# Kernel tuning notes

Measured on AMD Instinct MI355X. Metric: run time of the kernel, lower is better.

## Reference

```python
import jax, jax.numpy as jnp
import numpy as np

_SAMPLING_EPS = 1e-5


def setup_inputs() -> dict:
    key = jax.random.key(0)
    k1, k2, k3, k4, k5 = jax.random.split(key, 5)
    B, V = 128, 128000
    logits = jax.random.normal(k1, (B, V), dtype=jnp.float32)
    temperature = jax.random.uniform(k2, (B,), dtype=jnp.float32)
    top_k = jax.random.randint(k3, (B,), 0, 1024)
    top_p = jax.random.uniform(k4, (B,), dtype=jnp.float32)
    # uniform noise -> exponential via -log(u) inside reference (torch's q.exponential_())
    q = jnp.clip(jax.random.uniform(k5, (B, V), dtype=jnp.float32), 1e-10, 1.0)
    return {"logits": logits, "temperature": temperature, "top_k": top_k,
            "top_p": top_p, "q": q, "max_num_logprobs": 5}


def reference(logits, temperature, top_k, top_p, q, max_num_logprobs):
    B, V = logits.shape
    # apply_temperature: temp < eps treated as 1.0 (greedy rows untouched)
    temp = jnp.where(temperature < _SAMPLING_EPS, 1.0, temperature)
    logits = logits.astype(jnp.float32) / temp[:, None]

    # _apply_top_k_top_p: ascending sort over vocab
    idx = jnp.argsort(logits, axis=-1)                      # [B, V]
    ls = jnp.take_along_axis(logits, idx, axis=-1)          # sorted ascending
    k = jnp.clip(top_k.astype(jnp.int32), 1, V)
    thr = jnp.take_along_axis(ls, (V - k)[:, None], axis=-1)  # k-th largest value
    ls = jnp.where(ls < thr, -jnp.inf, ls)
    # top-p on the top-k-masked sorted logits
    ps = jax.nn.softmax(ls, axis=-1)
    cum = jnp.cumsum(ps, axis=-1)
    p_mask = cum <= (1.0 - top_p)[:, None]
    p_mask = p_mask.at[:, -1].set(False)
    ls = jnp.where(p_mask, -jnp.inf, ls)
    # scatter masked sorted logits back to original vocab positions
    rows = jnp.arange(B)[:, None]
    logits = jnp.zeros_like(logits).at[rows, idx].set(ls)

    # get_probs + sample
    probs = jax.nn.softmax(logits, axis=-1)
    e = -jnp.log(q)                                         # exponential noise
    greedy = jnp.argmax(probs, axis=-1)
    rand = jnp.argmax(probs / e, axis=-1)                   # Gumbel-max equivalent
    sampled = jnp.where(temperature < _SAMPLING_EPS, greedy, rand).astype(jnp.int32)

    # top-k logprobs
    logprobs = jax.nn.log_softmax(logits, axis=-1)
    topk_logprobs, topk_indices = jax.lax.top_k(logprobs, max_num_logprobs)
    return sampled, topk_logprobs, topk_indices.astype(jnp.int32)
```

## Files before the change

kernel.cpp:

```cpp
#include <hip/hip_runtime.h>
#include <math.h>
#include <float.h>

typedef unsigned long long u64;
typedef unsigned u32;

#define NT 1024
#define NW 16
#define NT1 256
#define SL 8
#define NB 8192
#define BSH 19
#define NBM 4096
#define CAP 2048
#define EPT4 8
#define SUB2 64
#define TOPN 5
#define SCALE_D 17592186044416.0
#define NEG_BIG -3.0e38f

#define ADDRT(g) ((((g) & 15u) << 8) | ((g) >> 4))

struct RowCtl { u32 kb; u32 cnt0; u32 maxKey; u32 rin; u32 bail; u32 pad[27]; };

__device__ __forceinline__ u32 key_of(float f){
  u32 u = __float_as_uint(f);
  return (u & 0x80000000u) ? ~u : (u | 0x80000000u);
}
__device__ __forceinline__ float key_to_float(u32 k){
  u32 u = (k & 0x80000000u) ? (k & 0x7FFFFFFFu) : ~k;
  return __uint_as_float(u);
}
__device__ __forceinline__ u64 quantMass(float l, float m){
  float ef = expf(l - m);
  return (u64)((double)ef * SCALE_D + 0.5);
}

struct Top5 { float v[TOPN]; int ix[TOPN]; };
__device__ __forceinline__ void t5_init(Top5& t){
  for (int j=0;j<TOPN;j++){ t.v[j] = -INFINITY; t.ix[j] = 0x7FFFFFFF; }
}
__device__ __forceinline__ void t5_insert(Top5& t, float nv, int ni){
  for (int j=0;j<TOPN;j++){
    if (nv > t.v[j] || (nv == t.v[j] && ni < t.ix[j])){
      for (int s=TOPN-1;s>j;s--){ t.v[s]=t.v[s-1]; t.ix[s]=t.ix[s-1]; }
      t.v[j]=nv; t.ix[j]=ni;
      return;
    }
  }
}

__device__ void scan_excl(u64* arr, int n, u64* wsum){
  const int tid = threadIdx.x, lane = tid & 63, w = tid >> 6;
  __syncthreads();
  const int chunk = (n + NT - 1) / NT;
  const int base = tid * chunk;
  u64 local = 0;
  for (int j=0;j<chunk;j++){ int i=base+j; if (i<n) local += arr[i]; }
  u64 inc = local;
  for (int off=1; off<64; off<<=1){
    u64 up = __shfl_up(inc, off, 64);
    if (lane >= off) inc += up;
  }
  if (lane == 63) wsum[w] = inc;
  __syncthreads();
  if (tid == 0){
    u64 acc = 0;
    for (int i=0;i<NW;i++){ u64 v = wsum[i]; wsum[i] = acc; acc += v; }
    arr[n] = acc;
  }
  __syncthreads();
  u64 run = wsum[w] + (inc - local);
  for (int j=0;j<chunk;j++){ int i=base+j; if (i<n){ u64 v=arr[i]; arr[i]=run; run += v; } }
  __syncthreads();
}


__global__ void k0_zero(u32* __restrict__ hist, u32* __restrict__ ctlw, int Bn){
  size_t n = (size_t)Bn * NB;
  size_t stride = (size_t)gridDim.x * blockDim.x;
  for (size_t i = (size_t)blockIdx.x*blockDim.x + threadIdx.x; i < n; i += stride) hist[i] = 0;
  size_t nc = (size_t)Bn * (sizeof(RowCtl)/4);
  for (size_t i = (size_t)blockIdx.x*blockDim.x + threadIdx.x; i < nc; i += stride) ctlw[i] = 0;
}

__global__ __launch_bounds__(NT1) void k1_hist(const float* __restrict__ L,
        const float* __restrict__ temp, u32* __restrict__ hist, RowCtl* __restrict__ ctl,
        int Bn, int Vn){
  __shared__ u32 lh[NB];
  const int b = blockIdx.y, s = blockIdx.x, tid = threadIdx.x;
  for (int j=tid;j<NB;j+=NT1) lh[j]=0;
  const float tr = temp[b]; const float tEff = (tr < 1e-5f) ? 1.0f : tr;
  const float* Lr = L + (size_t)b*Vn;
  const int chunk = (Vn + SL-1)/SL;
  const int i0 = s*chunk, i1 = min(i0+chunk, Vn);
  __syncthreads();
  const int nv = (i1 - i0) / 4;
  const float4* L4 = (const float4*)(Lr + i0);
  u32 mk = 0;
  for (int v=tid; v<nv; v+=NT1){
    float4 x = L4[v];
    #pragma unroll
    for (int e=0;e<4;e++){
      float l = (&x.x)[e] / tEff;
      u32 k = key_of(l);
      atomicAdd(&lh[k>>BSH], 1u);
      mk = max(mk, k);
    }
  }
  for (int i=i0+nv*4+tid; i<i1; i+=NT1){
    float l = Lr[i]/tEff;
    u32 k = key_of(l);
    atomicAdd(&lh[k>>BSH], 1u);
    mk = max(mk, k);
  }
  for (int off=32; off; off>>=1){ u32 o=__shfl_xor(mk,off,64); mk=max(mk,o); }
  if ((tid&63)==0) atomicMax(&ctl[b].maxKey, mk);
  __syncthreads();
  u32* Hr = hist + (size_t)b*NB;
  for (int j=tid;j<NB;j+=NT1){ u32 c = lh[j]; if (c) atomicAdd(&Hr[j], c); }
}

__global__ __launch_bounds__(NT) void k2_kb(const int* __restrict__ top_k,
        const u32* __restrict__ hist, RowCtl* __restrict__ ctl, int Bn, int Vn){
  __shared__ u32 sh[NB+1];
  __shared__ u32 wsum[NW];
  __shared__ int s_g;
  __shared__ u32 s_base;
  const int b = blockIdx.x, tid = threadIdx.x, lane = tid&63, w = tid>>6;
  const u32* Hr = hist + (size_t)b*NB;
  for (int j=tid;j<NB;j+=NT) sh[j] = Hr[j];
  __syncthreads();
  const int chunk = NB/NT;
  u32 local=0;
  for (int j=0;j<chunk;j++) local += sh[tid*chunk+j];
  u32 inc = local;
  for (int off=1;off<64;off<<=1){ u32 up=__shfl_up(inc,off,64); if (lane>=off) inc+=up; }
  if (lane==63) wsum[w]=inc;
  __syncthreads();
  if (tid==0){ u32 acc=0; for(int i=0;i<NW;i++){u32 v=wsum[i]; wsum[i]=acc; acc+=v;} sh[NB]=acc; }
  __syncthreads();
  u32 run = wsum[w] + (inc - local);
  for (int j=0;j<chunk;j++){ int i2=tid*chunk+j; u32 v=sh[i2]; sh[i2]=run; run+=v; }
  __syncthreads();
  int kk = top_k[b]; if (kk<1) kk=1; if (kk>Vn) kk=Vn;
  const u32 rank = (u32)(Vn - kk);
  for (int j=tid;j<NB;j+=NT) if (sh[j] <= rank && rank < sh[j+1]){ s_g = j; s_base = sh[j]; }
  __syncthreads();
  if (tid==0){ ctl[b].kb = (u32)s_g; ctl[b].rin = rank - s_base; }
}

__global__ __launch_bounds__(NT1) void k3_collect(const float* __restrict__ L,
        const float* __restrict__ temp, u64* __restrict__ cand, RowCtl* __restrict__ ctl,
        int Bn, int Vn){
  const int b = blockIdx.y, s = blockIdx.x, tid = threadIdx.x;
  const float tr = temp[b]; const float tEff = (tr<1e-5f)?1.0f:tr;
  const u32 kbMinKey = ctl[b].kb << BSH;
  const float* Lr = L + (size_t)b*Vn;
  u64* Cr = cand + (size_t)b*CAP;
  const int chunk = (Vn + SL-1)/SL;
  const int i0 = s*chunk, i1 = min(i0+chunk, Vn);
  const int nv = (i1 - i0) / 4;
  const float4* L4 = (const float4*)(Lr + i0);
  const int lane = tid & 63;
  for (int v=tid; v<nv; v+=NT1){
    float4 x = L4[v];
    #pragma unroll
    for (int e=0;e<4;e++){
      float l = (&x.x)[e] / tEff;
      u32 k = key_of(l);
      bool pred = (k >= kbMinKey);
      u64 mk = __ballot(pred);
      if (mk){
        int leader = __ffsll((long long)mk) - 1;
        u32 base = 0;
        if (lane == leader) base = atomicAdd(&ctl[b].cnt0, (u32)__popcll(mk));
        base = __shfl(base, leader, 64);
        if (pred){
          u32 p = base + (u32)__popcll(mk & ((1ull<<lane)-1ull));
          if (p < CAP) Cr[p] = ((u64)k<<32) | (u64)(u32)(i0 + v*4 + e);
        }
      }
    }
  }
  for (int i=i0+nv*4+tid; i<i1; i+=NT1){
    float l = Lr[i]/tEff;
    u32 k = key_of(l);
    if (k >= kbMinKey){
      u32 p = atomicAdd(&ctl[b].cnt0, 1u);
      if (p < CAP) Cr[p] = ((u64)k<<32) | (u64)(u32)i;
    }
  }
}

__global__ __launch_bounds__(NT1) void k4_solve(const float* __restrict__ L,
        const float* __restrict__ temp, const int* __restrict__ top_k,
        const float* __restrict__ top_p, const float* __restrict__ qn,
        const u64* __restrict__ cand, RowCtl* __restrict__ ctl,
        float* __restrict__ out, int Bn, int Vn){
  __shared__ u32 cnt[NBM];
  __shared__ u64 mass[NBM];
  __shared__ u64 sub[SUB2];
  __shared__ u64 msub[SUB2];
  __shared__ u32 wsc[4];
  __shared__ u64 wsm[4];
  __shared__ u64 s_ibs[4];
  __shared__ int s_cnt, s_bail, s_ga, s_gb;
  __shared__ u32 s_thr, s_r3;
  __shared__ float s_fill[16];
  __shared__ Top5 s_wt5[4];
  __shared__ double s_wr[4];
  __shared__ int s_wri[4], s_wg[4];
  __shared__ u64 s_ms[4], s_pb[4];

  const int b = blockIdx.x, tid = threadIdx.x, lane = tid&63, w = tid>>6;
  const u32 n0raw = ctl[b].cnt0;
  if (n0raw == 0 || n0raw > CAP) return;
  const int n0 = (int)n0raw;
  const float tr = temp[b]; const float tEff = (tr<1e-5f)?1.0f:tr;
  const float* Lr = L + (size_t)b*Vn;
  const float* Qr = qn + (size_t)b*Vn;
  const u64* Cr = cand + (size_t)b*CAP;
  const u32 kb = ctl[b].kb;
  const u32 rin = ctl[b].rin;
  const u32 mKey = ctl[b].maxKey;
  const u32 kbMin = kb << BSH;
  const float m = key_to_float(mKey);

  for (int i=tid;i<NBM;i+=NT1){ cnt[i]=0; mass[i]=0; }
  if (tid==0){ s_cnt=0; s_bail=0; s_ga=0; s_gb=0; s_r3=0; }
  if (tid<16) s_fill[tid] = (tid<Vn) ? Lr[tid] : 0.f;
  u64 pr[EPT4]; u32 kk_[EPT4]; bool vd[EPT4]; float qv[EPT4];
  #pragma unroll
  for (int e=0;e<EPT4;e++){
    int p = tid + e*NT1;
    vd[e] = (p < n0);
    pr[e] = vd[e] ? Cr[p] : ~0ull;
    kk_[e] = (u32)(pr[e]>>32);
  }
  #pragma unroll
  for (int e=0;e<EPT4;e++) qv[e] = vd[e] ? Qr[(u32)pr[e]] : 1.0f;

  const u32 span = mKey - kbMin;
  int shb = 0; if (span > 4095u){ int hb = 31 - __clz(span); shb = hb - 11; }
  u64 msA[EPT4]; u32 binA[EPT4], binM[EPT4]; bool inkb[EPT4];
  #pragma unroll
  for (int e=0;e<EPT4;e++){
    inkb[e] = vd[e] && ((kk_[e]>>BSH) == kb);
    binA[e] = (kk_[e] & 0x7FFFFu) >> 7;
    binM[e] = vd[e] ? ((kk_[e] - kbMin) >> shb) : 0u;
    msA[e]  = vd[e] ? quantMass(key_to_float(kk_[e]), m) : 0ull;
  }
  __syncthreads();
  #pragma unroll
  for (int e=0;e<EPT4;e++){
    if (inkb[e]) atomicAdd(&cnt[ADDRT(binA[e])], 1u);
    if (vd[e])   atomicAdd(&mass[ADDRT(binM[e])], msA[e]);
  }
  __syncthreads();

  u32 c16[16]; u64 m16[16];
  u32 lsc = 0; u64 lsm = 0;
  #pragma unroll
  for (int j=0;j<16;j++){
    c16[j] = cnt[(j<<8)|tid]; lsc += c16[j];
    m16[j] = mass[(j<<8)|tid]; lsm += m16[j];
  }
  u32 incc = lsc; u64 incm = lsm;
  for (int off=1;off<64;off<<=1){
    u32 uc=__shfl_up(incc,off,64); if (lane>=off) incc+=uc;
    u64 um=__shfl_up(incm,off,64); if (lane>=off) incm+=um;
  }
  if (lane==63){ wsc[w]=incc; wsm[w]=incm; }
  __syncthreads();
  u32 wbc=0; u64 wbm=0, Tall=0;
  for (int i=0;i<4;i++){ Tall += wsm[i]; if (i<w){ wbc += wsc[i]; wbm += wsm[i]; } }
  u32 runc = wbc + incc - lsc;
  const u64 runm = wbm + incm - lsm;
  u64 runm2 = runm;
  #pragma unroll
  for (int j=0;j<16;j++){
    if (runc <= rin && rin < runc + c16[j]){ s_ga = tid*16+j; s_r3 = rin - runc; }
    runc += c16[j];
    mass[(j<<8)|tid] = runm2;
    runm2 += m16[j];
  }
  __syncthreads();
  const int ga = s_ga; const u32 r3 = s_r3;
  #pragma unroll
  for (int e=0;e<EPT4;e++){
    if (inkb[e] && (int)binA[e] == ga){
      int p = atomicAdd(&s_cnt, 1);
      if (p < SUB2) sub[p] = pr[e]; else s_bail = 1;
    }
  }
  __syncthreads();
  if (s_bail){ if (tid==0) ctl[b].bail = 1; return; }
  const int ncolA = min(s_cnt, SUB2);
  for (int t=tid; t<ncolA; t+=NT1){
    u64 own = sub[t]; u32 rk = 0;
    for (int j=0;j<ncolA;j++) rk += (sub[j] < own);
    if (rk == r3) s_thr = (u32)(own>>32);
  }
  if (tid==0) s_cnt = 0;
  __syncthreads();
  const u32 thrKey = s_thr;
  const int thrBin = (int)((thrKey - kbMin) >> shb);

  u64 ibs = 0;
  #pragma unroll
  for (int e=0;e<EPT4;e++)
    if (vd[e] && (int)binM[e] == thrBin && kk_[e] >= thrKey) ibs += msA[e];
  for (int off=1;off<64;off<<=1) ibs += __shfl_xor(ibs, off, 64);
  if (lane==0) s_ibs[w] = ibs;
  __syncthreads();
  const u64 inB = s_ibs[0]+s_ibs[1]+s_ibs[2]+s_ibs[3];
  const u64 prefA = (thrBin >= NBM-1) ? Tall : mass[ADDRT((u32)(thrBin+1))];
  const u64 T = Tall - prefA + inB;
  const float cf = 1.0f - top_p[b];
  u64 Q = (u64)((double)cf * (double)T);
  if (Q >= T) Q = T - 1;
  const bool inThr = (Q < inB);
  const u64 Qp = Q + prefA - inB;
  if (!inThr){
    u64 run3 = runm;
    #pragma unroll
    for (int j=0;j<16;j++){
      if (run3 <= Qp && Qp < run3 + m16[j]) s_gb = tid*16+j;
      run3 += m16[j];
    }
  } else if (tid==0) s_gb = thrBin;
  __syncthreads();
  const int gb = s_gb;
  const u64 Pgb = inThr ? 0ull : mass[ADDRT((u32)gb)];
  const u64 Qd  = inThr ? Q : Qp;
  #pragma unroll
  for (int e=0;e<EPT4;e++){
    bool f = vd[e] && ((int)binM[e] == gb) && (!inThr || kk_[e] >= thrKey);
    if (f){
      int p = atomicAdd(&s_cnt, 1);
      if (p < SUB2){ sub[p] = pr[e]; msub[p] = msA[e]; } else s_bail = 1;
    }
  }
  __syncthreads();
  if (s_bail){ if (tid==0) ctl[b].bail = 1; return; }
  const int ncolB = min(s_cnt, SUB2);
  u64 cacc[EPT4]; bool inb[EPT4];
  #pragma unroll
  for (int e=0;e<EPT4;e++){
    inb[e] = vd[e] && ((int)binM[e] == gb) && (!inThr || kk_[e] >= thrKey);
    cacc[e] = 0;
  }
  for (int j=0;j<ncolB;j++){
    u64 pj = sub[j]; u64 mj = msub[j];
    #pragma unroll
    for (int e=0;e<EPT4;e++)
      if (inb[e] && pj < pr[e]) cacc[e] += mj;
  }
  bool sv[EPT4]; u64 mm = 0; u64 pb = ~0ull;
  #pragma unroll
  for (int e=0;e<EPT4;e++){
    bool isSurvKey = vd[e] && kk_[e] >= thrKey;
    bool masked = false;
    if (isSurvKey){
      if ((int)binM[e] < gb) masked = true;
      else if (inb[e] && (Pgb + cacc[e] + msA[e]) <= Qd) masked = true;
    }
    sv[e] = isSurvKey && !masked;
    if (isSurvKey && masked) mm += msA[e];
    if (sv[e] && pr[e] < pb) pb = pr[e];
  }

  Top5 t5; t5_init(t5);
  double br = -1.0; int bri = 0x7FFFFFFF; int gmin = 0x7FFFFFFF;
  #pragma unroll
  for (int e=0;e<EPT4;e++){
    if (sv[e]){
      float l = key_to_float(kk_[e]); int idx = (int)(u32)pr[e];
      double ratio = (double)expf(l - m) / (double)(-logf(qv[e]));
      if (ratio > br || (ratio == br && idx < bri)){ br = ratio; bri = idx; }
      if (kk_[e] == mKey && idx < gmin) gmin = idx;
      t5_insert(t5, l, idx);
    }
  }
  for (int off=1; off<64; off<<=1){
    Top5 o;
    for (int j=0;j<TOPN;j++){ o.v[j]=__shfl_xor(t5.v[j],off,64); o.ix[j]=__shfl_xor(t5.ix[j],off,64); }
    for (int j=0;j<TOPN;j++) t5_insert(t5, o.v[j], o.ix[j]);
    double orr = __shfl_xor(br, off, 64); int ori = __shfl_xor(bri, off, 64);
    if (orr > br || (orr == br && ori < bri)){ br = orr; bri = ori; }
    int og = __shfl_xor(gmin, off, 64); if (og < gmin) gmin = og;
    mm += __shfl_xor(mm, off, 64);
    u64 op = __shfl_xor(pb, off, 64); if (op < pb) pb = op;
  }
  if (lane==0){ s_wt5[w]=t5; s_wr[w]=br; s_wri[w]=bri; s_wg[w]=gmin; s_ms[w]=mm; s_pb[w]=pb; }
  __syncthreads();
  if (tid==0){
    Top5 f = s_wt5[0];
    double fr = s_wr[0]; int fri = s_wri[0]; int fg = s_wg[0];
    u64 fms = s_ms[0]; u64 fpb = s_pb[0];
    for (int wi=1; wi<4; wi++){
      for (int j=0;j<TOPN;j++) t5_insert(f, s_wt5[wi].v[j], s_wt5[wi].ix[j]);
      if (s_wr[wi] > fr || (s_wr[wi]==fr && s_wri[wi]<fri)){ fr=s_wr[wi]; fri=s_wri[wi]; }
      if (s_wg[wi] < fg) fg = s_wg[wi];
      fms += s_ms[wi];
      if (s_pb[wi] < fpb) fpb = s_pb[wi];
    }
    const u64 S2 = T - fms;
    int filled = 0;
    for (int i=0; i<16 && i<Vn && filled<TOPN; i++){
      float l = s_fill[i]/tEff;
      u64 pr2 = ((u64)key_of(l)<<32) | (u64)(u32)i;
      if (pr2 < fpb){ t5_insert(f, -INFINITY, i); filled++; }
    }
    double lS = log((double)S2 / SCALE_D);
    int sampled = (tr < 1e-5f) ? fg : fri;
    out[b] = (float)sampled;
    for (int j=0;j<TOPN;j++){
      float lv = f.v[j];
      float lp = (lv == -INFINITY) ? NEG_BIG : (float)((double)lv - (double)m - lS);
      out[Bn + b*TOPN + j] = lp;
      out[Bn + Bn*TOPN + b*TOPN + j] = (float)f.ix[j];
    }
  }
}


__device__ void find_cross(const u64* arr, int n, u64 target, int* s_fh, u64* s_fb){
  const int tid = threadIdx.x;
  const int chunk = (n + NT - 1) / NT;
  const int base = tid * chunk;
  for (int j=0;j<chunk;j++){
    int i = base + j;
    if (i < n && arr[i] <= target && target < arr[i+1]){ *s_fh = i; *s_fb = arr[i]; }
  }
  __syncthreads();
}

__device__ void fallback_row(int b, const float* logits, const float* temperature,
                             const int* top_k, const float* top_p, const float* qnoise,
                             float* out, int Bn, int Vn){
  __shared__ u64 s_hist[4097];
  __shared__ u64 s_wsum[NW];
  __shared__ int s_fh;
  __shared__ u64 s_fb;
  __shared__ float s_fm[NW];
  __shared__ float s_m;
  __shared__ int s_lastMax;
  __shared__ int s_eqcnt;
  __shared__ int s_eqlist[1024];
  __shared__ int s_sel;
  __shared__ Top5 s_wt5[NW];
  __shared__ double s_wr[NW];
  __shared__ int s_wri[NW];
  __shared__ int s_wg[NW];
  __shared__ u64 s_ws2[NW];

  const int tid = threadIdx.x, lane = tid & 63, w = tid >> 6;
  const float* L  = logits + (size_t)b * Vn;
  const float* Qr = qnoise + (size_t)b * Vn;
  const float tRaw = temperature[b];
  const float tEff = (tRaw < 1e-5f) ? 1.0f : tRaw;

  for (int i=tid;i<4097;i+=NT) s_hist[i] = 0;
  if (tid==0){ s_lastMax = -1; s_eqcnt = 0; }
  __syncthreads();
  float lm = -INFINITY;
  for (int i=tid;i<Vn;i+=NT){
    float l = L[i] / tEff;
    u32 k = key_of(l);
    atomicAdd(&s_hist[k>>20], 1ull);
    lm = fmaxf(lm, l);
  }
  for (int off=32; off; off>>=1) lm = fmaxf(lm, __shfl_xor(lm, off, 64));
  if (lane==0) s_fm[w] = lm;
  scan_excl(s_hist, 4096, s_wsum);
  if (tid==0){ float mm=-INFINITY; for (int i=0;i<NW;i++) mm=fmaxf(mm,s_fm[i]); s_m=mm; }
  __syncthreads();
  const float m = s_m;

  int kk = top_k[b]; if (kk < 1) kk = 1; if (kk > Vn) kk = Vn;
  u64 r = (u64)(Vn - kk);
  find_cross(s_hist, 4096, r, &s_fh, &s_fb);
  const int kb0 = s_fh; r -= s_fb;
  __syncthreads();

  for (int i=tid;i<4097;i+=NT) s_hist[i]=0;
  __syncthreads();
  for (int i=tid;i<Vn;i+=NT){
    float l = L[i]/tEff; u32 k = key_of(l);
    if ((int)(k>>20) == kb0) atomicAdd(&s_hist[(k>>8)&0xFFFu], 1ull);
  }
  scan_excl(s_hist, 4096, s_wsum);
  find_cross(s_hist, 4096, r, &s_fh, &s_fb);
  const int kb1 = s_fh; r -= s_fb;
  __syncthreads();

  const u32 ktop24 = ((u32)kb0<<12) | (u32)kb1;
  for (int i=tid;i<4097;i+=NT) s_hist[i]=0;
  __syncthreads();
  for (int i=tid;i<Vn;i+=NT){
    float l = L[i]/tEff; u32 k = key_of(l);
    if ((k>>8) == ktop24) atomicAdd(&s_hist[k & 0xFFu], 1ull);
  }
  scan_excl(s_hist, 256, s_wsum);
  find_cross(s_hist, 256, r, &s_fh, &s_fb);
  const u32 thrKey = (ktop24<<8) | (u32)s_fh;
  const float thr = key_to_float(thrKey);
  __syncthreads();

  for (int i=tid;i<4097;i+=NT) s_hist[i]=0;
  __syncthreads();
  for (int i=tid;i<Vn;i+=NT){
    float l = L[i]/tEff;
    if (l >= thr){
      u32 k = key_of(l);
      double sd = exp((double)l - (double)m);
      u64 qv = (u64)(sd * SCALE_D + 0.5);
      atomicAdd(&s_hist[k>>20], qv);
      if (l == m) atomicMax(&s_lastMax, i);
    }
  }
  scan_excl(s_hist, 4096, s_wsum);
  const u64 T = s_hist[4096];
  const float cf = 1.0f - top_p[b];
  const double qtd = (double)cf * (double)T;
  u64 Qfix = (qtd >= (double)T) ? T : (u64)qtd;
  const bool allmask = (Qfix >= T);

  u32 vKey = 0xFFFFFFFFu;
  int idxStar = 0x7FFFFFFF;

  if (!allmask){
    find_cross(s_hist, 4096, Qfix, &s_fh, &s_fb);
    const int g0 = s_fh;
    u64 Qrem = Qfix - s_fb;
    __syncthreads();

    for (int i=tid;i<4097;i+=NT) s_hist[i]=0;
    __syncthreads();
    for (int i=tid;i<Vn;i+=NT){
      float l = L[i]/tEff;
      if (l >= thr){
        u32 k = key_of(l);
        if ((int)(k>>20) == g0){
          double sd = exp((double)l - (double)m);
          atomicAdd(&s_hist[(k>>8)&0xFFFu], (u64)(sd*SCALE_D+0.5));
        }
      }
    }
    scan_excl(s_hist, 4096, s_wsum);
    find_cross(s_hist, 4096, Qrem, &s_fh, &s_fb);
    const int g1 = s_fh; Qrem -= s_fb;
    __syncthreads();

    const u32 ptop24 = ((u32)g0<<12)|(u32)g1;
    for (int i=tid;i<4097;i+=NT) s_hist[i]=0;
    __syncthreads();
    for (int i=tid;i<Vn;i+=NT){
      float l = L[i]/tEff;
      if (l >= thr){
        u32 k = key_of(l);
        if ((k>>8) == ptop24){
          double sd = exp((double)l - (double)m);
          atomicAdd(&s_hist[k & 0xFFu], (u64)(sd*SCALE_D+0.5));
        }
      }
    }
    scan_excl(s_hist, 256, s_wsum);
    find_cross(s_hist, 256, Qrem, &s_fh, &s_fb);
    const int g2 = s_fh;
    const u64 base2 = s_fb;
    const u64 nextPref = s_hist[g2+1];
    Qrem -= base2;
    vKey = (ptop24<<8) | (u32)g2;
    const float vStar = key_to_float(vKey);
    const double sv = exp((double)vStar - (double)m);
    const u64 qstar = (u64)(sv*SCALE_D+0.5);
    u64 nstar = (qstar > 0) ? (nextPref - base2) / qstar : 1ull;
    if (nstar < 1) nstar = 1;
    u64 tmask = (qstar > 0) ? (Qrem / qstar) : 0ull;
    if (tmask >= nstar) tmask = nstar - 1;
    idxStar = -1;
    __syncthreads();
    if (tmask >= 1){
      for (int i=tid;i<Vn;i+=NT){
        float l = L[i]/tEff;
        if (key_of(l) == vKey){
          int p = atomicAdd(&s_eqcnt, 1);
          if (p < 1024) s_eqlist[p] = i;
        }
      }
      __syncthreads();
      if (tid == 0){
        int n_ = s_eqcnt; if (n_ > 1024) n_ = 1024;
        for (int a=1;a<n_;a++){
          int key0 = s_eqlist[a]; int c2=a-1;
          while (c2>=0 && s_eqlist[c2]>key0){ s_eqlist[c2+1]=s_eqlist[c2]; c2--; }
          s_eqlist[c2+1]=key0;
        }
        int ti = (int)tmask - 1;
        if (ti >= n_) ti = n_-1;
        s_sel = s_eqlist[ti];
      }
      __syncthreads();
      idxStar = s_sel;
    }
  }

  const int lastMax = s_lastMax;
  Top5 t5; t5_init(t5);
  u64 s2 = 0;
  double br = -1.0; int bri = 0x7FFFFFFF;
  int gmin = 0x7FFFFFFF;
  for (int i=tid;i<Vn;i+=NT){
    float l = L[i]/tEff;
    u32 k = key_of(l);
    bool surv = (l >= thr) &&
                ((k > vKey) || (k == vKey && i > idxStar) || (i == lastMax));
    float val;
    if (surv){
      double sd = exp((double)l - (double)m);
      s2 += (u64)(sd*SCALE_D+0.5);
      float u = expf(l - m);
      float e = -logf(Qr[i]);
      double ratio = (double)u / (double)e;
      if (ratio > br || (ratio == br && i < bri)){ br = ratio; bri = i; }
      if (l == m && i < gmin) gmin = i;
      val = l;
    } else {
      val = -INFINITY;
    }
    t5_insert(t5, val, i);
  }
  for (int off=1; off<64; off<<=1){
    Top5 o;
    for (int j=0;j<TOPN;j++){ o.v[j]=__shfl_xor(t5.v[j],off,64); o.ix[j]=__shfl_xor(t5.ix[j],off,64); }
    for (int j=0;j<TOPN;j++) t5_insert(t5, o.v[j], o.ix[j]);
    double orr = __shfl_xor(br, off, 64);
    int ori = __shfl_xor(bri, off, 64);
    if (orr > br || (orr == br && ori < bri)){ br = orr; bri = ori; }
    int og = __shfl_xor(gmin, off, 64); if (og < gmin) gmin = og;
    s2 += __shfl_xor(s2, off, 64);
  }
  if (lane == 0){
    s_wt5[w] = t5; s_wr[w]=br; s_wri[w]=bri; s_wg[w]=gmin; s_ws2[w]=s2;
  }
  __syncthreads();
  if (tid == 0){
    Top5 f = s_wt5[0];
    double fr = s_wr[0]; int fri = s_wri[0]; int fg = s_wg[0];
    u64 fs2 = s_ws2[0];
    for (int wi=1; wi<NW; wi++){
      for (int j=0;j<TOPN;j++) t5_insert(f, s_wt5[wi].v[j], s_wt5[wi].ix[j]);
      if (s_wr[wi] > fr || (s_wr[wi]==fr && s_wri[wi]<fri)){ fr=s_wr[wi]; fri=s_wri[wi]; }
      if (s_wg[wi] < fg) fg = s_wg[wi];
      fs2 += s_ws2[wi];
    }
    double S2d = (double)fs2 / SCALE_D;
    double lS = log(S2d);
    int sampled = (tRaw < 1e-5f) ? fg : fri;
    out[b] = (float)sampled;
    for (int j=0;j<TOPN;j++){
      float lv = f.v[j];
      float lp = (lv == -INFINITY) ? NEG_BIG : (float)((double)lv - (double)m - lS);
      out[Bn + b*TOPN + j] = lp;
      out[Bn + Bn*TOPN + b*TOPN + j] = (float)f.ix[j];
    }
  }
}

__global__ __launch_bounds__(NT) void k5_rowfb(const float* __restrict__ logits,
        const float* __restrict__ temperature, const int* __restrict__ top_k,
        const float* __restrict__ top_p, const float* __restrict__ qnoise,
        const RowCtl* __restrict__ ctl, float* __restrict__ out, int Bn, int Vn){
  const int b = blockIdx.x;
  const u32 c = ctl[b].cnt0;
  if (c > 0 && c <= CAP && !ctl[b].bail) return;
  fallback_row(b, logits, temperature, top_k, top_p, qnoise, out, Bn, Vn);
}

extern "C" __global__ void __launch_bounds__(NT)
sampler_fallback(const float* __restrict__ logits, const float* __restrict__ temperature,
                 const int* __restrict__ top_k, const float* __restrict__ top_p,
                 const float* __restrict__ qnoise, float* __restrict__ out, int Bn, int Vn){
  fallback_row(blockIdx.x, logits, temperature, top_k, top_p, qnoise, out, Bn, Vn);
}


extern "C" void kernel_launch(void* const* d_in, const int* in_sizes, int n_in,
                              void* d_out, int out_size, void* d_ws, size_t ws_size,
                              hipStream_t stream)
{
  const float* logits      = (const float*)d_in[0];
  const float* temperature = (const float*)d_in[1];
  const int*   top_k       = (const int*)d_in[2];
  const float* top_p       = (const float*)d_in[3];
  const float* q           = (const float*)d_in[4];
  const int Bn = in_sizes[1];
  const int Vn = in_sizes[0] / Bn;

  const size_t offCand = (size_t)Bn * NB * 4;
  const size_t offCtl  = offCand + (size_t)Bn * CAP * 8;
  const size_t total   = offCtl + (size_t)Bn * sizeof(RowCtl);

  if (ws_size < total){
    sampler_fallback<<<dim3(Bn), dim3(NT), 0, stream>>>(
        logits, temperature, top_k, top_p, q, (float*)d_out, Bn, Vn);
    return;
  }

  char* wsb = (char*)d_ws;
  u32*    hist = (u32*)wsb;
  u64*    cand = (u64*)(wsb + offCand);
  RowCtl* ctl  = (RowCtl*)(wsb + offCtl);

  k0_zero   <<<dim3(512),     dim3(256), 0, stream>>>(hist, (u32*)ctl, Bn);
  k1_hist   <<<dim3(SL, Bn),  dim3(NT1), 0, stream>>>(logits, temperature, hist, ctl, Bn, Vn);
  k2_kb     <<<dim3(Bn),      dim3(NT),  0, stream>>>(top_k, hist, ctl, Bn, Vn);
  k3_collect<<<dim3(SL, Bn),  dim3(NT1), 0, stream>>>(logits, temperature, cand, ctl, Bn, Vn);
  k4_solve  <<<dim3(Bn),      dim3(NT1), 0, stream>>>(logits, temperature, top_k, top_p, q,
                                                      cand, ctl, (float*)d_out, Bn, Vn);
  k5_rowfb  <<<dim3(Bn),      dim3(NT),  0, stream>>>(logits, temperature, top_k, top_p, q,
                                                      ctl, (float*)d_out, Bn, Vn);
}
```

Baseline: 132.2 us.

## Fuse histogram prefix-scan threshold search into candidate collection kernel

Removes the separate k2_kb launch by having every collect block load the row histogram, do a padded-LDS transposed prefix scan over 256 threads, and locate the top-k bucket itself before filtering candidates. This saves one kernel launch and its dependency gap, at the cost of redundant scanning in each of the SL blocks per row and about 33KB of extra LDS per block, which may reduce occupancy. Only block 0 of each row writes kb and rin to the control struct for later kernels.

```diff
diff --git a/kernel.cpp b/kernel.cpp
--- a/kernel.cpp
+++ b/kernel.cpp
@@ -20,6 +20,7 @@
 #define NEG_BIG -3.0e38f
 
 #define ADDRT(g) ((((g) & 15u) << 8) | ((g) >> 4))
+#define ADDRP(g) (((g) & 31u) * 257u + ((g) >> 5))
 
 struct RowCtl { u32 kb; u32 cnt0; u32 maxKey; u32 rin; u32 bail; u32 pad[27]; };
 
@@ -121,48 +122,49 @@
   for (int j=tid;j<NB;j+=NT1){ u32 c = lh[j]; if (c) atomicAdd(&Hr[j], c); }
 }
 
-__global__ __launch_bounds__(NT) void k2_kb(const int* __restrict__ top_k,
-        const u32* __restrict__ hist, RowCtl* __restrict__ ctl, int Bn, int Vn){
-  __shared__ u32 sh[NB+1];
-  __shared__ u32 wsum[NW];
-  __shared__ int s_g;
-  __shared__ u32 s_base;
-  const int b = blockIdx.x, tid = threadIdx.x, lane = tid&63, w = tid>>6;
+__global__ __launch_bounds__(NT1) void k3_collect(const float* __restrict__ L,
+        const float* __restrict__ temp, const int* __restrict__ top_k,
+        const u32* __restrict__ hist, u64* __restrict__ cand, RowCtl* __restrict__ ctl,
+        int Bn, int Vn){
+  __shared__ u32 lh2[32*257];
+  __shared__ u32 wsk[4];
+  __shared__ int s_kb;
+  __shared__ u32 s_rin;
+  const int b = blockIdx.y, s = blockIdx.x, tid = threadIdx.x;
+  const int lane = tid & 63, w = tid >> 6;
+  const float tr = temp[b]; const float tEff = (tr<1e-5f)?1.0f:tr;
+  const float* Lr = L + (size_t)b*Vn;
+  u64* Cr = cand + (size_t)b*CAP;
+
   const u32* Hr = hist + (size_t)b*NB;
-  for (int j=tid;j<NB;j+=NT) sh[j] = Hr[j];
-  __syncthreads();
-  const int chunk = NB/NT;
-  u32 local=0;
-  for (int j=0;j<chunk;j++) local += sh[tid*chunk+j];
-  u32 inc = local;
-  for (int off=1;off<64;off<<=1){ u32 up=__shfl_up(inc,off,64); if (lane>=off) inc+=up; }
-  if (lane==63) wsum[w]=inc;
-  __syncthreads();
-  if (tid==0){ u32 acc=0; for(int i=0;i<NW;i++){u32 v=wsum[i]; wsum[i]=acc; acc+=v;} sh[NB]=acc; }
-  __syncthreads();
-  u32 run = wsum[w] + (inc - local);
-  for (int j=0;j<chunk;j++){ int i2=tid*chunk+j; u32 v=sh[i2]; sh[i2]=run; run+=v; }
-  __syncthreads();
+  for (int i=tid; i<NB; i+=NT1) lh2[ADDRP((u32)i)] = Hr[i];
+  __syncthreads();
+  u32 c32[32]; u32 lsum = 0;
+  #pragma unroll
+  for (int j=0;j<32;j++){ c32[j] = lh2[(u32)j*257u + (u32)tid]; lsum += c32[j]; }
+  u32 inc = lsum;
+  for (int off=1; off<64; off<<=1){ u32 up=__shfl_up(inc,off,64); if (lane>=off) inc+=up; }
+  if (lane==63) wsk[w] = inc;
+  __syncthreads();
+  u32 wb = 0;
+  for (int i=0;i<4;i++) if (i<w) wb += wsk[i];
+  u32 run = wb + inc - lsum;
   int kk = top_k[b]; if (kk<1) kk=1; if (kk>Vn) kk=Vn;
   const u32 rank = (u32)(Vn - kk);
-  for (int j=tid;j<NB;j+=NT) if (sh[j] <= rank && rank < sh[j+1]){ s_g = j; s_base = sh[j]; }
-  __syncthreads();
-  if (tid==0){ ctl[b].kb = (u32)s_g; ctl[b].rin = rank - s_base; }
-}
-
-__global__ __launch_bounds__(NT1) void k3_collect(const float* __restrict__ L,
-        const float* __restrict__ temp, u64* __restrict__ cand, RowCtl* __restrict__ ctl,
-        int Bn, int Vn){
-  const int b = blockIdx.y, s = blockIdx.x, tid = threadIdx.x;
-  const float tr = temp[b]; const float tEff = (tr<1e-5f)?1.0f:tr;
-  const u32 kbMinKey = ctl[b].kb << BSH;
-  const float* Lr = L + (size_t)b*Vn;
-  u64* Cr = cand + (size_t)b*CAP;
+  #pragma unroll
+  for (int j=0;j<32;j++){
+    if (run <= rank && rank < run + c32[j]){ s_kb = tid*32+j; s_rin = rank - run; }
+    run += c32[j];
+  }
+  __syncthreads();
+  const u32 kb = (u32)s_kb;
+  const u32 kbMinKey = kb << BSH;
+  if (s == 0 && tid == 0){ ctl[b].kb = kb; ctl[b].rin = s_rin; }
+
   const int chunk = (Vn + SL-1)/SL;
   const int i0 = s*chunk, i1 = min(i0+chunk, Vn);
   const int nv = (i1 - i0) / 4;
   const float4* L4 = (const float4*)(Lr + i0);
-  const int lane = tid & 63;
   for (int v=tid; v<nv; v+=NT1){
     float4 x = L4[v];
     #pragma unroll
@@ -717,8 +719,8 @@
 
   k0_zero   <<<dim3(512),     dim3(256), 0, stream>>>(hist, (u32*)ctl, Bn);
   k1_hist   <<<dim3(SL, Bn),  dim3(NT1), 0, stream>>>(logits, temperature, hist, ctl, Bn, Vn);
-  k2_kb     <<<dim3(Bn),      dim3(NT),  0, stream>>>(top_k, hist, ctl, Bn, Vn);
-  k3_collect<<<dim3(SL, Bn),  dim3(NT1), 0, stream>>>(logits, temperature, cand, ctl, Bn, Vn);
+  k3_collect<<<dim3(SL, Bn),  dim3(NT1), 0, stream>>>(logits, temperature, top_k, hist,
+                                                      cand, ctl, Bn, Vn);
   k4_solve  <<<dim3(Bn),      dim3(NT1), 0, stream>>>(logits, temperature, top_k, top_p, q,
                                                       cand, ctl, (float*)d_out, Bn, Vn);
   k5_rowfb  <<<dim3(Bn),      dim3(NT),  0, stream>>>(logits, temperature, top_k, top_p, q,
```

Measured after the change: 133.8 us. About the same (+1.2%).
